# Performance work log

Measured on AMD Instinct MI355X. Metric: run time of the kernel, lower is better.

Reference implementation:

```python
import jax, jax.numpy as jnp
import numpy as np

NT, C, B, N, H, E = 32768, 128, 64, 512, 4, 524288  # total nodes, channels, graphs, nodes/graph, heads, edges
DH = C // H
EPS = 1e-5


def batchnorm(x, g, b):
    # BatchNorm1d over the node dimension (training-mode batch statistics)
    m = x.mean(axis=0)
    v = x.var(axis=0)
    return (x - m) * jax.lax.rsqrt(v + EPS) * g + b


def setup_inputs() -> dict:
    key = jax.random.key(0)
    ks = jax.random.split(key, 8)
    s = 1.0 / np.sqrt(C)
    return dict(
        x=jax.random.normal(ks[0], (NT, C), jnp.float32),
        edge_index=jax.random.randint(ks[1], (2, E), 0, NT, dtype=jnp.int32),
        Wc=jax.random.normal(ks[2], (C, C), jnp.float32) * s,
        bc=jnp.zeros((C,), jnp.float32),
        in_proj_w=jax.random.normal(ks[3], (3 * C, C), jnp.float32) * s,
        in_proj_b=jnp.zeros((3 * C,), jnp.float32),
        out_proj_w=jax.random.normal(ks[4], (C, C), jnp.float32) * s,
        out_proj_b=jnp.zeros((C,), jnp.float32),
        gn1=jnp.ones((C,), jnp.float32), bn1=jnp.zeros((C,), jnp.float32),
        gn2=jnp.ones((C,), jnp.float32), bn2=jnp.zeros((C,), jnp.float32),
        gn3=jnp.ones((C,), jnp.float32), bn3=jnp.zeros((C,), jnp.float32),
        Wm1=jax.random.normal(ks[5], (2 * C, C), jnp.float32) * s,
        bm1=jnp.zeros((2 * C,), jnp.float32),
        Wm2=jax.random.normal(ks[6], (C, 2 * C), jnp.float32) / np.sqrt(2 * C),
        bm2=jnp.zeros((C,), jnp.float32),
    )


def reference(x, edge_index, Wc, bc, in_proj_w, in_proj_b, out_proj_w, out_proj_b,
              gn1, bn1, gn2, bn2, gn3, bn3, Wm1, bm1, Wm2, bm2):
    # --- local branch: mean-aggregation message passing + linear + residual + BN ---
    src, dst = edge_index[0], edge_index[1]
    agg = jax.ops.segment_sum(x[src], dst, num_segments=NT)            # [NT, C]
    cnt = jax.ops.segment_sum(jnp.ones((E, 1), x.dtype), dst, num_segments=NT)
    agg = agg / jnp.maximum(cnt, 1.0)
    h_local = agg @ Wc.T + bc + x                                       # dropout p=0 -> no-op
    h_local = batchnorm(h_local, gn1, bn1)

    # --- global branch: to_dense_batch (equal-size graphs -> reshape) + MHA ---
    hd = x.reshape(B, N, C)
    qkv = hd @ in_proj_w.T + in_proj_b                                  # [B, N, 3C]
    q, k, v = jnp.split(qkv, 3, axis=-1)
    q = q.reshape(B, N, H, DH).transpose(0, 2, 1, 3)                    # [B, H, N, DH]
    k = k.reshape(B, N, H, DH).transpose(0, 2, 1, 3)
    v = v.reshape(B, N, H, DH).transpose(0, 2, 1, 3)
    scores = jnp.einsum('bhqd,bhkd->bhqk', q, k) / np.sqrt(DH)          # [B, H, N, N]
    attn = jax.nn.softmax(scores, axis=-1)
    o = jnp.einsum('bhqk,bhkd->bhqd', attn, v)                          # [B, H, N, DH]
    o = o.transpose(0, 2, 1, 3).reshape(B, N, C)
    h_attn = (o @ out_proj_w.T + out_proj_b).reshape(NT, C) + x
    h_attn = batchnorm(h_attn, gn2, bn2)

    # --- combine + MLP + final norm ---
    out = h_local + h_attn
    out = out + (jax.nn.relu(out @ Wm1.T + bm1) @ Wm2.T + bm2)
    return batchnorm(out, gn3, bn3)
```

## Files before the change

kernel.cpp:

```cpp
#include <hip/hip_runtime.h>
#include <cstddef>

#define NT    32768
#define CCH   128
#define BB    64
#define NNODE 512
#define NHEAD 4
#define DHEAD 32
#define EE    524288
#define EPS   1e-5f
#define MAXDEG 96
#define CURPAD 16
#define SSLOT  8
#define EGRP  2048

typedef unsigned short u16;
typedef unsigned int   u32;
typedef __attribute__((ext_vector_type(8))) short short8;
typedef __attribute__((ext_vector_type(4))) short short4v;
typedef __attribute__((ext_vector_type(4))) float f32x4;

__device__ __forceinline__ float b2f(u32 w) { return __uint_as_float(w << 16); }
__device__ __forceinline__ u16 f2b(float f) {
    u32 u = __float_as_uint(f);
    u += 0x7FFF + ((u >> 16) & 1);
    return (u16)(u >> 16);
}

__global__ __launch_bounds__(256) void prep_kernel(const float* __restrict__ x,
                                                   const float* __restrict__ Wc,
                                                   const float* __restrict__ Wqkv,
                                                   const float* __restrict__ Wo,
                                                   const float* __restrict__ Wm1,
                                                   const float* __restrict__ Wm2,
                                                   u16* __restrict__ xb,
                                                   u16* __restrict__ Wcb,
                                                   u16* __restrict__ Wqkvb,
                                                   u16* __restrict__ Wob,
                                                   u16* __restrict__ Wm1b,
                                                   u16* __restrict__ Wm2b,
                                                   const int* __restrict__ ei,
                                                   int* __restrict__ cursor,
                                                   int* __restrict__ bucket) {
    if (blockIdx.x >= 2120) {
        int b2 = blockIdx.x - 2120;
        int k = b2 & 7;
        int g = b2 >> 3;
        int base_e = g * EGRP;
        for (int j = threadIdx.x; j < EGRP; j += 256) {
            int dst = ei[EE + base_e + j];
            if ((dst & 7) == k) {
                int src = ei[base_e + j];
                int pos = atomicAdd(cursor + dst * CURPAD, 1);
                if (pos < MAXDEG) bucket[dst * MAXDEG + pos] = src;
            }
        }
        return;
    }
    int r = blockIdx.x * 256 + threadIdx.x;
    const float* src; u16* dst;
    if (r < 524288) { src = x; dst = xb; }
    else if ((r -= 524288) < 2048) { src = Wc; dst = Wcb; }
    else if ((r -= 2048) < 6144) { src = Wqkv; dst = Wqkvb; }
    else if ((r -= 6144) < 2048) { src = Wo; dst = Wob; }
    else if ((r -= 2048) < 4096) { src = Wm1; dst = Wm1b; }
    else { r -= 4096; src = Wm2; dst = Wm2b; }
    size_t base = (size_t)r * 8;
    float4 a = *(const float4*)(src + base);
    float4 b = *(const float4*)(src + base + 4);
    uint4 u;
    u.x = (u32)f2b(a.x) | ((u32)f2b(a.y) << 16);
    u.y = (u32)f2b(a.z) | ((u32)f2b(a.w) << 16);
    u.z = (u32)f2b(b.x) | ((u32)f2b(b.y) << 16);
    u.w = (u32)f2b(b.z) | ((u32)f2b(b.w) << 16);
    *(uint4*)(dst + base) = u;
}

struct GemmSmem {
    u16 As[128 * 32];
    u16 Bs[128 * 32];
    u16 Cs[4][16 * 72];
    float csum[128];
    float csq[128];
};

template <bool RELU, int RESID, bool STATS>
__device__ __forceinline__ void gemm_body(u16* __restrict__ As, u16* __restrict__ Bs,
                                          u16* __restrict__ Cs0, float* __restrict__ csum,
                                          float* __restrict__ csq,
                                          const u16* __restrict__ A,
                                          const u16* __restrict__ W,
                                          const float* __restrict__ bias,
                                          const u16* __restrict__ residb,
                                          u16* __restrict__ outb, int ostride,
                                          float* __restrict__ sum, float* __restrict__ sumsq,
                                          int slotbase, int m0, int K) {
    int tid = threadIdx.x;
    int lane = tid & 63, wave = tid >> 6;
    int wm = (wave & 1) * 64, wn = (wave >> 1) * 64;
    int l15 = lane & 15, l4 = lane >> 4;
    u16* Csw = Cs0 + wave * (16 * 72);

    if (STATS) {
        if (tid < 128) { csum[tid] = 0.f; csq[tid] = 0.f; }
    }

    f32x4 zero = {0.f, 0.f, 0.f, 0.f};
    f32x4 acc[4][4];
#pragma unroll
    for (int i = 0; i < 4; ++i)
#pragma unroll
        for (int j = 0; j < 4; ++j) acc[i][j] = zero;

    int srow = tid >> 2;
    int scol = (tid & 3) * 8;

    int kIter = K >> 5;
    uint4 a0 = *(const uint4*)(A + (size_t)(m0 + srow) * K + scol);
    uint4 a1 = *(const uint4*)(A + (size_t)(m0 + srow + 64) * K + scol);
    uint4 b0 = *(const uint4*)(W + (size_t)srow * K + scol);
    uint4 b1 = *(const uint4*)(W + (size_t)(srow + 64) * K + scol);
    for (int ki = 0; ki < kIter; ++ki) {
        if (ki) __syncthreads();
        *(uint4*)&As[srow * 32 + scol] = a0;
        *(uint4*)&As[(srow + 64) * 32 + scol] = a1;
        *(uint4*)&Bs[srow * 32 + scol] = b0;
        *(uint4*)&Bs[(srow + 64) * 32 + scol] = b1;
        if (ki + 1 < kIter) {
            int k0 = (ki + 1) * 32;
            a0 = *(const uint4*)(A + (size_t)(m0 + srow) * K + k0 + scol);
            a1 = *(const uint4*)(A + (size_t)(m0 + srow + 64) * K + k0 + scol);
            b0 = *(const uint4*)(W + (size_t)srow * K + k0 + scol);
            b1 = *(const uint4*)(W + (size_t)(srow + 64) * K + k0 + scol);
        }
        __syncthreads();
        short8 af[4], bf[4];
#pragma unroll
        for (int t = 0; t < 4; ++t) {
            af[t] = *(const short8*)&As[(wm + t * 16 + l15) * 32 + l4 * 8];
            bf[t] = *(const short8*)&Bs[(wn + t * 16 + l15) * 32 + l4 * 8];
        }
#pragma unroll
        for (int mt = 0; mt < 4; ++mt)
#pragma unroll
            for (int nt = 0; nt < 4; ++nt)
                acc[mt][nt] = __builtin_amdgcn_mfma_f32_16x16x32_bf16(af[mt], bf[nt], acc[mt][nt], 0, 0, 0);
    }

    float ps[4] = {0.f, 0.f, 0.f, 0.f};
    float pq[4] = {0.f, 0.f, 0.f, 0.f};
    int rl = lane >> 3;
    int cg = lane & 7;
#pragma unroll
    for (int mt = 0; mt < 4; ++mt) {
#pragma unroll
        for (int nt = 0; nt < 4; ++nt) {
            int lcol = wn + nt * 16 + l15;
            float bs = bias[lcol];
#pragma unroll
            for (int r = 0; r < 4; ++r) {
                int row = m0 + wm + mt * 16 + l4 * 4 + r;
                float v = acc[mt][nt][r] + bs;
                if (RESID == 2) v += b2f(residb[(size_t)row * 128 + lcol]);
                if (RELU) v = fmaxf(v, 0.0f);
                Csw[(l4 * 4 + r) * 72 + nt * 16 + l15] = f2b(v);
                if (STATS) { ps[nt] += v; pq[nt] += v * v; }
            }
        }
#pragma unroll
        for (int p = 0; p < 2; ++p) {
            int lrow = p * 8 + rl;
            uint4 wv = *(const uint4*)&Csw[lrow * 72 + cg * 8];
            int grow = m0 + wm + mt * 16 + lrow;
            *(uint4*)(outb + (size_t)grow * ostride + wn + cg * 8) = wv;
        }
    }
    if (STATS) {
#pragma unroll
        for (int nt = 0; nt < 4; ++nt) {
            atomicAdd(&csum[wn + nt * 16 + l15], ps[nt]);
            atomicAdd(&csq[wn + nt * 16 + l15], pq[nt]);
        }
        __syncthreads();
        if (tid < 128) {
            atomicAdd(sum + slotbase + tid, csum[tid]);
            atomicAdd(sumsq + slotbase + tid, csq[tid]);
        }
    }
}

__global__ __launch_bounds__(256) void gemm_wc_qkv(const int* __restrict__ bucket,
                                                   const int* __restrict__ cursor,
                                                   const u16* __restrict__ Wcb,
                                                   const float* __restrict__ bc,
                                                   const u16* __restrict__ xb,
                                                   u16* __restrict__ aggb,
                                                   u16* __restrict__ hlocb,
                                                   float* __restrict__ sum1,
                                                   float* __restrict__ sq1,
                                                   const u16* __restrict__ Wqkvb,
                                                   const float* __restrict__ bqkv,
                                                   u16* __restrict__ qkvb) {
    __shared__ GemmSmem sm;
    int y = blockIdx.y;
    int m0 = blockIdx.x * 128;
    int tid = threadIdx.x;

    if (y != 0) {
        gemm_body<false, 0, false>(sm.As, sm.Bs, &sm.Cs[0][0], sm.csum, sm.csq,
                                   xb, Wqkvb + (size_t)(y - 1) * 16384,
                                   bqkv + (y - 1) * 128, nullptr,
                                   qkvb + (y - 1) * 128, 384, nullptr, nullptr, 0, m0, 128);
        return;
    }

    {
        int (*srcs)[MAXDEG] = reinterpret_cast<int (*)[MAXDEG]>(sm.As);
        int ln = tid >> 4;
        int c8 = tid & 15;
        const u16* xp = xb + c8 * 8;
        for (int pass = 0; pass < 8; ++pass) {
            int n = pass * 16 + ln;
            int gn = m0 + n;
            int d = min(cursor[gn * CURPAD], MAXDEG);
            for (int j = c8; j < d; j += 16) srcs[ln][j] = bucket[gn * MAXDEG + j];
            __syncthreads();
            float s[8] = {0.f, 0.f, 0.f, 0.f, 0.f, 0.f, 0.f, 0.f};
            for (int base = 0; base < d; base += 8) {
                uint4 w[8];
#pragma unroll
                for (int u = 0; u < 8; ++u) {
                    int jj = base + u;
                    int idx = srcs[ln][jj < d ? jj : 0];
                    w[u] = *(const uint4*)(xp + (size_t)idx * CCH);
                }
#pragma unroll
                for (int u = 0; u < 8; ++u) {
                    if (base + u >= d) { w[u].x = 0; w[u].y = 0; w[u].z = 0; w[u].w = 0; }
                    s[0] += b2f(w[u].x & 0xffffu);
                    s[1] += b2f(w[u].x >> 16);
                    s[2] += b2f(w[u].y & 0xffffu);
                    s[3] += b2f(w[u].y >> 16);
                    s[4] += b2f(w[u].z & 0xffffu);
                    s[5] += b2f(w[u].z >> 16);
                    s[6] += b2f(w[u].w & 0xffffu);
                    s[7] += b2f(w[u].w >> 16);
                }
            }
            float inv = 1.0f / fmaxf((float)d, 1.0f);
            uint4 out;
            out.x = (u32)f2b(s[0] * inv) | ((u32)f2b(s[1] * inv) << 16);
            out.y = (u32)f2b(s[2] * inv) | ((u32)f2b(s[3] * inv) << 16);
            out.z = (u32)f2b(s[4] * inv) | ((u32)f2b(s[5] * inv) << 16);
            out.w = (u32)f2b(s[6] * inv) | ((u32)f2b(s[7] * inv) << 16);
            *(uint4*)(aggb + (size_t)gn * CCH + c8 * 8) = out;
            __syncthreads();
        }
    }
    __syncthreads();

    gemm_body<false, 2, true>(sm.As, sm.Bs, &sm.Cs[0][0], sm.csum, sm.csq,
                              aggb, Wcb, bc, xb, hlocb, 128, sum1, sq1,
                              (blockIdx.x & (SSLOT - 1)) << 7, m0, 128);
}

__global__ __launch_bounds__(256) void gemm_wo(const u16* __restrict__ ob,
                                               const u16* __restrict__ Wob,
                                               const float* __restrict__ bo,
                                               const u16* __restrict__ xb,
                                               u16* __restrict__ t2b,
                                               float* __restrict__ sum2, float* __restrict__ sq2) {
    __shared__ GemmSmem sm;
    gemm_body<false, 2, true>(sm.As, sm.Bs, &sm.Cs[0][0], sm.csum, sm.csq,
                              ob, Wob, bo, xb, t2b, 128, sum2, sq2,
                              (blockIdx.x & (SSLOT - 1)) << 7, blockIdx.x * 128, 128);
}

__global__ __launch_bounds__(256) void gemm_mlp2(const u16* __restrict__ hidb,
                                                 const u16* __restrict__ Wm2b,
                                                 const float* __restrict__ bm2,
                                                 const u16* __restrict__ shb,
                                                 u16* __restrict__ out2b,
                                                 float* __restrict__ sum3, float* __restrict__ sq3) {
    __shared__ GemmSmem sm;
    gemm_body<false, 2, true>(sm.As, sm.Bs, &sm.Cs[0][0], sm.csum, sm.csq,
                              hidb, Wm2b, bm2, shb, out2b, 128, sum3, sq3,
                              (blockIdx.x & (SSLOT - 1)) << 7, blockIdx.x * 128, 256);
}

__global__ __launch_bounds__(256) void gemm_m1c(const u16* __restrict__ hlocb,
                                                const u16* __restrict__ t2b,
                                                const float* __restrict__ sum1,
                                                const float* __restrict__ sq1,
                                                const float* __restrict__ g1,
                                                const float* __restrict__ bt1,
                                                const float* __restrict__ sum2,
                                                const float* __restrict__ sq2,
                                                const float* __restrict__ g2,
                                                const float* __restrict__ bt2,
                                                u16* __restrict__ shb,
                                                const u16* __restrict__ Wm1b,
                                                const float* __restrict__ bm1,
                                                u16* __restrict__ hidb) {
    __shared__ u16 As[128 * 32];
    __shared__ u16 Bs[128 * 32];
    __shared__ u16 Cs[4][16 * 72];
    __shared__ float AF1[128], BF1[128], AF2[128], BF2[128];
    int tid = threadIdx.x;
    {
        int c = tid & 127;
        const float* sm = (tid < 128) ? sum1 : sum2;
        const float* sq = (tid < 128) ? sq1 : sq2;
        const float* g  = (tid < 128) ? g1 : g2;
        const float* bt = (tid < 128) ? bt1 : bt2;
        float s = 0.f, q = 0.f;
#pragma unroll
        for (int sl = 0; sl < SSLOT; ++sl) { s += sm[sl * 128 + c]; q += sq[sl * 128 + c]; }
        float m = s * (1.0f / NT);
        float v = q * (1.0f / NT) - m * m;
        float a = g[c] * rsqrtf(v + EPS);
        if (tid < 128) { AF1[c] = a; BF1[c] = bt[c] - m * a; }
        else           { AF2[c] = a; BF2[c] = bt[c] - m * a; }
    }
    int m0 = blockIdx.x * 128, n0 = blockIdx.y * 128;
    int lane = tid & 63, wave = tid >> 6;
    int wm = (wave & 1) * 64, wn = (wave >> 1) * 64;
    int l15 = lane & 15, l4 = lane >> 4;

    f32x4 zero = {0.f, 0.f, 0.f, 0.f};
    f32x4 acc[4][4];
#pragma unroll
    for (int i = 0; i < 4; ++i)
#pragma unroll
        for (int j = 0; j < 4; ++j) acc[i][j] = zero;

    int srow = tid >> 2;
    int scol = (tid & 3) * 8;
    bool wr = (blockIdx.y == 0);

    uint4 h0 = *(const uint4*)(hlocb + (size_t)(m0 + srow) * 128 + scol);
    uint4 h1 = *(const uint4*)(hlocb + (size_t)(m0 + srow + 64) * 128 + scol);
    uint4 t0 = *(const uint4*)(t2b + (size_t)(m0 + srow) * 128 + scol);
    uint4 t1 = *(const uint4*)(t2b + (size_t)(m0 + srow + 64) * 128 + scol);
    uint4 b0 = *(const uint4*)(Wm1b + (size_t)(n0 + srow) * 128 + scol);
    uint4 b1 = *(const uint4*)(Wm1b + (size_t)(n0 + srow + 64) * 128 + scol);
    __syncthreads();
    for (int ki = 0; ki < 4; ++ki) {
        int k0 = ki * 32;
        if (ki) __syncthreads();
        uint4 c0, c1;
        {
            const u32 hw[4] = {h0.x, h0.y, h0.z, h0.w};
            const u32 tw[4] = {t0.x, t0.y, t0.z, t0.w};
            u32 ow[4];
#pragma unroll
            for (int p = 0; p < 4; ++p) {
                int cc = k0 + scol + p * 2;
                float v0 = AF1[cc] * b2f(hw[p] & 0xffffu) + BF1[cc] + AF2[cc] * b2f(tw[p] & 0xffffu) + BF2[cc];
                float v1 = AF1[cc + 1] * b2f(hw[p] >> 16) + BF1[cc + 1] + AF2[cc + 1] * b2f(tw[p] >> 16) + BF2[cc + 1];
                ow[p] = (u32)f2b(v0) | ((u32)f2b(v1) << 16);
            }
            c0.x = ow[0]; c0.y = ow[1]; c0.z = ow[2]; c0.w = ow[3];
        }
        {
            const u32 hw[4] = {h1.x, h1.y, h1.z, h1.w};
            const u32 tw[4] = {t1.x, t1.y, t1.z, t1.w};
            u32 ow[4];
#pragma unroll
            for (int p = 0; p < 4; ++p) {
                int cc = k0 + scol + p * 2;
                float v0 = AF1[cc] * b2f(hw[p] & 0xffffu) + BF1[cc] + AF2[cc] * b2f(tw[p] & 0xffffu) + BF2[cc];
                float v1 = AF1[cc + 1] * b2f(hw[p] >> 16) + BF1[cc + 1] + AF2[cc + 1] * b2f(tw[p] >> 16) + BF2[cc + 1];
                ow[p] = (u32)f2b(v0) | ((u32)f2b(v1) << 16);
            }
            c1.x = ow[0]; c1.y = ow[1]; c1.z = ow[2]; c1.w = ow[3];
        }
        *(uint4*)&As[srow * 32 + scol] = c0;
        *(uint4*)&As[(srow + 64) * 32 + scol] = c1;
        *(uint4*)&Bs[srow * 32 + scol] = b0;
        *(uint4*)&Bs[(srow + 64) * 32 + scol] = b1;
        if (wr) {
            *(uint4*)(shb + (size_t)(m0 + srow) * 128 + k0 + scol) = c0;
            *(uint4*)(shb + (size_t)(m0 + srow + 64) * 128 + k0 + scol) = c1;
        }
        if (ki < 3) {
            int kn = k0 + 32;
            h0 = *(const uint4*)(hlocb + (size_t)(m0 + srow) * 128 + kn + scol);
            h1 = *(const uint4*)(hlocb + (size_t)(m0 + srow + 64) * 128 + kn + scol);
            t0 = *(const uint4*)(t2b + (size_t)(m0 + srow) * 128 + kn + scol);
            t1 = *(const uint4*)(t2b + (size_t)(m0 + srow + 64) * 128 + kn + scol);
            b0 = *(const uint4*)(Wm1b + (size_t)(n0 + srow) * 128 + kn + scol);
            b1 = *(const uint4*)(Wm1b + (size_t)(n0 + srow + 64) * 128 + kn + scol);
        }
        __syncthreads();
        short8 af[4], bf[4];
#pragma unroll
        for (int t = 0; t < 4; ++t) {
            af[t] = *(const short8*)&As[(wm + t * 16 + l15) * 32 + l4 * 8];
            bf[t] = *(const short8*)&Bs[(wn + t * 16 + l15) * 32 + l4 * 8];
        }
#pragma unroll
        for (int mt = 0; mt < 4; ++mt)
#pragma unroll
            for (int nt = 0; nt < 4; ++nt)
                acc[mt][nt] = __builtin_amdgcn_mfma_f32_16x16x32_bf16(af[mt], bf[nt], acc[mt][nt], 0, 0, 0);
    }

    int rl = lane >> 3;
    int cg = lane & 7;
#pragma unroll
    for (int mt = 0; mt < 4; ++mt) {
#pragma unroll
        for (int nt = 0; nt < 4; ++nt) {
            int col = n0 + wn + nt * 16 + l15;
            float bs = bm1[col];
#pragma unroll
            for (int r = 0; r < 4; ++r) {
                float v = fmaxf(acc[mt][nt][r] + bs, 0.0f);
                Cs[wave][(l4 * 4 + r) * 72 + nt * 16 + l15] = f2b(v);
            }
        }
#pragma unroll
        for (int p = 0; p < 2; ++p) {
            int lrow = p * 8 + rl;
            uint4 wv = *(const uint4*)&Cs[wave][lrow * 72 + cg * 8];
            int grow = m0 + wm + mt * 16 + lrow;
            *(uint4*)(hidb + (size_t)grow * 256 + n0 + wn + cg * 8) = wv;
        }
    }
}

__global__ __launch_bounds__(256) void final_bn(const u16* __restrict__ X,
                                                const float* __restrict__ sum3,
                                                const float* __restrict__ sq3,
                                                const float* __restrict__ g3,
                                                const float* __restrict__ bt3,
                                                float* __restrict__ outp) {
    __shared__ float A3[128], B3[128];
    int t = threadIdx.x;
    if (t < 128) {
        float s = 0.f, q = 0.f;
#pragma unroll
        for (int sl = 0; sl < SSLOT; ++sl) { s += sum3[sl * 128 + t]; q += sq3[sl * 128 + t]; }
        float m = s * (1.0f / NT);
        float v = q * (1.0f / NT) - m * m;
        float a = g3[t] * rsqrtf(v + EPS);
        A3[t] = a;
        B3[t] = bt3[t] - m * a;
    }
    __syncthreads();
    int i8 = blockIdx.x * 256 + t;
    size_t i = (size_t)i8 * 8;
    int c = (int)(i & (CCH - 1));
    uint4 u = *(const uint4*)(X + i);
    float x[8];
    x[0] = b2f(u.x & 0xffffu); x[1] = b2f(u.x >> 16);
    x[2] = b2f(u.y & 0xffffu); x[3] = b2f(u.y >> 16);
    x[4] = b2f(u.z & 0xffffu); x[5] = b2f(u.z >> 16);
    x[6] = b2f(u.w & 0xffffu); x[7] = b2f(u.w >> 16);
    float4 o0, o1;
    o0.x = A3[c + 0] * x[0] + B3[c + 0];
    o0.y = A3[c + 1] * x[1] + B3[c + 1];
    o0.z = A3[c + 2] * x[2] + B3[c + 2];
    o0.w = A3[c + 3] * x[3] + B3[c + 3];
    o1.x = A3[c + 4] * x[4] + B3[c + 4];
    o1.y = A3[c + 5] * x[5] + B3[c + 5];
    o1.z = A3[c + 6] * x[6] + B3[c + 6];
    o1.w = A3[c + 7] * x[7] + B3[c + 7];
    *(float4*)(outp + i) = o0;
    *(float4*)(outp + i + 4) = o1;
}

__global__ __launch_bounds__(512) void attn_mfma(const u16* __restrict__ qkv,
                                                 u16* __restrict__ o) {
    __shared__ __align__(16) u16 Ks[512 * 40];
    __shared__ __align__(16) u16 Vt[32 * 520];
    int bh = blockIdx.x;
    int b = bh >> 2, h = bh & 3;
    int tid = threadIdx.x;
    int lane = tid & 63, wave = tid >> 6;
    int quad = lane >> 4, l15 = lane & 15;
    const float scale = 0.1767766952966369f;

    const u16* kvbase = qkv + (size_t)b * 512 * 384 + 128 + h * 32;
    for (int idx = tid; idx < 2048; idx += 512) {
        int row = idx >> 2, c = idx & 3;
        *(uint4*)&Ks[row * 40 + c * 8] = *(const uint4*)(kvbase + (size_t)row * 384 + c * 8);
    }
    for (int idx = tid; idx < 2048; idx += 512) {
        int row = idx >> 2, c = idx & 3;
        uint4 u = *(const uint4*)(kvbase + 128 + (size_t)row * 384 + c * 8);
        u16 e[8];
        *(uint4*)e = u;
#pragma unroll
        for (int i = 0; i < 8; ++i) Vt[(c * 8 + i) * 520 + row] = e[i];
    }
    __syncthreads();

    f32x4 zero = {0.f, 0.f, 0.f, 0.f};
    for (int qt = 0; qt < 4; ++qt) {
        int qbase = wave * 64 + qt * 16;
        short8 qf = *(const short8*)(qkv + (size_t)(b * 512 + qbase + l15) * 384 + h * 32 + quad * 8);
        float lq = 0.f;
        f32x4 oa[2] = {zero, zero};

        for (int kv0 = 0; kv0 < 512; kv0 += 64) {
            f32x4 s[4];
#pragma unroll
            for (int t = 0; t < 4; ++t) {
                short8 kb = *(const short8*)&Ks[(kv0 + t * 16 + l15) * 40 + quad * 8];
                s[t] = __builtin_amdgcn_mfma_f32_16x16x32_bf16(kb, qf, zero, 0, 0, 0);
            }
            short8 pp[2];
#pragma unroll
            for (int t = 0; t < 4; ++t) {
                float p0 = __expf(s[t][0] * scale);
                float p1 = __expf(s[t][1] * scale);
                float p2 = __expf(s[t][2] * scale);
                float p3 = __expf(s[t][3] * scale);
                lq += (p0 + p1) + (p2 + p3);
                int hi = (t & 1) * 4;
                pp[t >> 1][hi + 0] = (short)f2b(p0);
                pp[t >> 1][hi + 1] = (short)f2b(p1);
                pp[t >> 1][hi + 2] = (short)f2b(p2);
                pp[t >> 1][hi + 3] = (short)f2b(p3);
            }
#pragma unroll
            for (int tp = 0; tp < 2; ++tp) {
                int tb = kv0 + tp * 32;
#pragma unroll
                for (int n = 0; n < 2; ++n) {
                    const u16* vrow = &Vt[(n * 16 + l15) * 520 + tb + quad * 4];
                    short4v va = *(const short4v*)vrow;
                    short4v vb2 = *(const short4v*)(vrow + 16);
                    short8 vv = {va.x, va.y, va.z, va.w, vb2.x, vb2.y, vb2.z, vb2.w};
                    oa[n] = __builtin_amdgcn_mfma_f32_16x16x32_bf16(pp[tp], vv, oa[n], 0, 0, 0);
                }
            }
        }
        lq += __shfl_xor(lq, 16);
        lq += __shfl_xor(lq, 32);
        u16* op = o + (size_t)(b * 512 + qbase) * 128 + h * 32;
#pragma unroll
        for (int r = 0; r < 4; ++r) {
            float Lr = __shfl(lq, quad * 4 + r);
            float inv = 1.0f / Lr;
#pragma unroll
            for (int n = 0; n < 2; ++n)
                op[(quad * 4 + r) * 128 + n * 16 + l15] = f2b(oa[n][r] * inv);
        }
    }
}

extern "C" void kernel_launch(void* const* d_in, const int* in_sizes, int n_in,
                              void* d_out, int out_size, void* d_ws, size_t ws_size,
                              hipStream_t stream) {
    const float* x    = (const float*)d_in[0];
    const int*   ei   = (const int*)d_in[1];
    const float* Wc   = (const float*)d_in[2];
    const float* bc   = (const float*)d_in[3];
    const float* Wqkv = (const float*)d_in[4];
    const float* bqkv = (const float*)d_in[5];
    const float* Wo   = (const float*)d_in[6];
    const float* bo   = (const float*)d_in[7];
    const float* gn1  = (const float*)d_in[8];
    const float* bn1b = (const float*)d_in[9];
    const float* gn2  = (const float*)d_in[10];
    const float* bn2b = (const float*)d_in[11];
    const float* gn3  = (const float*)d_in[12];
    const float* bn3b = (const float*)d_in[13];
    const float* Wm1  = (const float*)d_in[14];
    const float* bm1  = (const float*)d_in[15];
    const float* Wm2  = (const float*)d_in[16];
    const float* bm2  = (const float*)d_in[17];
    float* outp = (float*)d_out;

    char* w = (char*)d_ws;
    const size_t MB = 1024 * 1024;
    u16* xb    = (u16*)(w);
    u16* hlocb = (u16*)(w + 8 * MB);
    u16* t2b   = (u16*)(w + 16 * MB);
    u16* out2b = (u16*)(w + 24 * MB);
    u16* qkvb  = (u16*)(w + 32 * MB);
    u16* hidb  = (u16*)(w + 56 * MB);
    u16* shb   = (u16*)(w + 72 * MB);
    int* bucket = (int*)(w + 80 * MB);
    int* cursor = (int*)(w + 92 * MB);
    float* stats = (float*)(w + 94 * MB);
    u16* Wcb   = (u16*)(w + 95 * MB);
    u16* Wqkvb = Wcb + 16384;
    u16* Wob   = Wqkvb + 49152;
    u16* Wm1b  = Wob + 16384;
    u16* Wm2b  = Wm1b + 32768;
    u16* ob    = (u16*)(w + 96 * MB);
    float* sum1 = stats;                  float* sq1 = stats + 1024;
    float* sum2 = stats + 2048;           float* sq2 = stats + 3072;
    float* sum3 = stats + 4096;           float* sq3 = stats + 5120;

    hipMemsetAsync(cursor, 0, 2 * MB + 6 * 1024 * 4, stream);

    prep_kernel<<<2120 + 2048, 256, 0, stream>>>(x, Wc, Wqkv, Wo, Wm1, Wm2,
                                                 xb, Wcb, Wqkvb, Wob, Wm1b, Wm2b,
                                                 ei, cursor, bucket);

    {
        dim3 g(NT / 128, 4);
        gemm_wc_qkv<<<g, 256, 0, stream>>>(bucket, cursor, Wcb, bc, xb, shb, hlocb, sum1, sq1,
                                           Wqkvb, bqkv, qkvb);
    }

    attn_mfma<<<BB * NHEAD, 512, 0, stream>>>(qkvb, ob);

    gemm_wo<<<NT / 128, 256, 0, stream>>>(ob, Wob, bo, xb, t2b, sum2, sq2);

    {
        dim3 g(NT / 128, 2);
        gemm_m1c<<<g, 256, 0, stream>>>(hlocb, t2b, sum1, sq1, gn1, bn1b,
                                        sum2, sq2, gn2, bn2b, shb, Wm1b, bm1, hidb);
    }

    gemm_mlp2<<<NT / 128, 256, 0, stream>>>(hidb, Wm2b, bm2, shb, out2b, sum3, sq3);

    final_bn<<<NT * CCH / 8 / 256, 256, 0, stream>>>(out2b, sum3, sq3, gn3, bn3b, outp);
}
```

Measured before the change: 232.7 us.

## Co-schedule attention with neighbor aggregation and Wc GEMM in one launch

```diff
diff --git a/kernel.cpp b/kernel.cpp
--- a/kernel.cpp
+++ b/kernel.cpp
@@ -189,33 +189,122 @@
     }
 }
 
-__global__ __launch_bounds__(256) void gemm_wc_qkv(const int* __restrict__ bucket,
-                                                   const int* __restrict__ cursor,
-                                                   const u16* __restrict__ Wcb,
-                                                   const float* __restrict__ bc,
-                                                   const u16* __restrict__ xb,
-                                                   u16* __restrict__ aggb,
-                                                   u16* __restrict__ hlocb,
-                                                   float* __restrict__ sum1,
-                                                   float* __restrict__ sq1,
-                                                   const u16* __restrict__ Wqkvb,
-                                                   const float* __restrict__ bqkv,
-                                                   u16* __restrict__ qkvb) {
+__global__ __launch_bounds__(256) void gemm_qkv(const u16* __restrict__ xb,
+                                                const u16* __restrict__ Wqkvb,
+                                                const float* __restrict__ bqkv,
+                                                u16* __restrict__ qkvb) {
     __shared__ GemmSmem sm;
     int y = blockIdx.y;
-    int m0 = blockIdx.x * 128;
+    gemm_body<false, 0, false>(sm.As, sm.Bs, &sm.Cs[0][0], sm.csum, sm.csq,
+                               xb, Wqkvb + (size_t)y * 16384, bqkv + y * 128, nullptr,
+                               qkvb + y * 128, 384, nullptr, nullptr, 0, blockIdx.x * 128, 128);
+}
+
+struct K3Smem {
+    union {
+        struct { u16 Ks[512 * 40]; u16 Vt[32 * 520]; } a;
+        GemmSmem g;
+    };
+};
+
+__global__ __launch_bounds__(256) void attn_gwc(const u16* __restrict__ qkv,
+                                                u16* __restrict__ o,
+                                                const int* __restrict__ bucket,
+                                                const int* __restrict__ cursor,
+                                                const u16* __restrict__ Wcb,
+                                                const float* __restrict__ bc,
+                                                const u16* __restrict__ xb,
+                                                u16* __restrict__ aggb,
+                                                u16* __restrict__ hlocb,
+                                                float* __restrict__ sum1,
+                                                float* __restrict__ sq1) {
+    __shared__ __align__(16) K3Smem sm;
+    int bid = blockIdx.x;
     int tid = threadIdx.x;
 
-    if (y != 0) {
-        gemm_body<false, 0, false>(sm.As, sm.Bs, &sm.Cs[0][0], sm.csum, sm.csq,
-                                   xb, Wqkvb + (size_t)(y - 1) * 16384,
-                                   bqkv + (y - 1) * 128, nullptr,
-                                   qkvb + (y - 1) * 128, 384, nullptr, nullptr, 0, m0, 128);
+    if (bid < 256) {
+        u16* Ks = sm.a.Ks;
+        u16* Vt = sm.a.Vt;
+        int b = bid >> 2, h = bid & 3;
+        int lane = tid & 63, wave = tid >> 6;
+        int quad = lane >> 4, l15 = lane & 15;
+        const float scale = 0.1767766952966369f;
+
+        const u16* kvbase = qkv + (size_t)b * 512 * 384 + 128 + h * 32;
+        for (int idx = tid; idx < 2048; idx += 256) {
+            int row = idx >> 2, c = idx & 3;
+            *(uint4*)&Ks[row * 40 + c * 8] = *(const uint4*)(kvbase + (size_t)row * 384 + c * 8);
+        }
+        for (int idx = tid; idx < 2048; idx += 256) {
+            int row = idx >> 2, c = idx & 3;
+            uint4 u = *(const uint4*)(kvbase + 128 + (size_t)row * 384 + c * 8);
+            u16 e[8];
+            *(uint4*)e = u;
+#pragma unroll
+            for (int i = 0; i < 8; ++i) Vt[(c * 8 + i) * 520 + row] = e[i];
+        }
+        __syncthreads();
+
+        f32x4 zero = {0.f, 0.f, 0.f, 0.f};
+        for (int qt = 0; qt < 8; ++qt) {
+            int qbase = wave * 128 + qt * 16;
+            short8 qf = *(const short8*)(qkv + (size_t)(b * 512 + qbase + l15) * 384 + h * 32 + quad * 8);
+            float lq = 0.f;
+            f32x4 oa[2] = {zero, zero};
+
+            for (int kv0 = 0; kv0 < 512; kv0 += 64) {
+                f32x4 s[4];
+#pragma unroll
+                for (int t = 0; t < 4; ++t) {
+                    short8 kb = *(const short8*)&Ks[(kv0 + t * 16 + l15) * 40 + quad * 8];
+                    s[t] = __builtin_amdgcn_mfma_f32_16x16x32_bf16(kb, qf, zero, 0, 0, 0);
+                }
+                short8 pp[2];
+#pragma unroll
+                for (int t = 0; t < 4; ++t) {
+                    float p0 = __expf(s[t][0] * scale);
+                    float p1 = __expf(s[t][1] * scale);
+                    float p2 = __expf(s[t][2] * scale);
+                    float p3 = __expf(s[t][3] * scale);
+                    lq += (p0 + p1) + (p2 + p3);
+                    int hi = (t & 1) * 4;
+                    pp[t >> 1][hi + 0] = (short)f2b(p0);
+                    pp[t >> 1][hi + 1] = (short)f2b(p1);
+                    pp[t >> 1][hi + 2] = (short)f2b(p2);
+                    pp[t >> 1][hi + 3] = (short)f2b(p3);
+                }
+#pragma unroll
+                for (int tp = 0; tp < 2; ++tp) {
+                    int tb = kv0 + tp * 32;
+#pragma unroll
+                    for (int n = 0; n < 2; ++n) {
+                        const u16* vrow = &Vt[(n * 16 + l15) * 520 + tb + quad * 4];
+                        short4v va = *(const short4v*)vrow;
+                        short4v vb2 = *(const short4v*)(vrow + 16);
+                        short8 vv = {va.x, va.y, va.z, va.w, vb2.x, vb2.y, vb2.z, vb2.w};
+                        oa[n] = __builtin_amdgcn_mfma_f32_16x16x32_bf16(pp[tp], vv, oa[n], 0, 0, 0);
+                    }
+                }
+            }
+            lq += __shfl_xor(lq, 16);
+            lq += __shfl_xor(lq, 32);
+            u16* op = o + (size_t)(b * 512 + qbase) * 128 + h * 32;
+#pragma unroll
+            for (int r = 0; r < 4; ++r) {
+                float Lr = __shfl(lq, quad * 4 + r);
+                float inv = 1.0f / Lr;
+#pragma unroll
+                for (int n = 0; n < 2; ++n)
+                    op[(quad * 4 + r) * 128 + n * 16 + l15] = f2b(oa[n][r] * inv);
+            }
+        }
         return;
     }
 
+    int m0 = (bid - 256) * 128;
+
     {
-        int (*srcs)[MAXDEG] = reinterpret_cast<int (*)[MAXDEG]>(sm.As);
+        int (*srcs)[MAXDEG] = reinterpret_cast<int (*)[MAXDEG]>(sm.g.As);
         int ln = tid >> 4;
         int c8 = tid & 15;
         const u16* xp = xb + c8 * 8;
@@ -259,9 +348,9 @@
     }
     __syncthreads();
 
-    gemm_body<false, 2, true>(sm.As, sm.Bs, &sm.Cs[0][0], sm.csum, sm.csq,
+    gemm_body<false, 2, true>(sm.g.As, sm.g.Bs, &sm.g.Cs[0][0], sm.g.csum, sm.g.csq,
                               aggb, Wcb, bc, xb, hlocb, 128, sum1, sq1,
-                              (blockIdx.x & (SSLOT - 1)) << 7, m0, 128);
+                              ((bid - 256) & (SSLOT - 1)) << 7, m0, 128);
 }
 
 __global__ __launch_bounds__(256) void gemm_wo(const u16* __restrict__ ob,
@@ -471,87 +560,6 @@
     *(float4*)(outp + i + 4) = o1;
 }
 
-__global__ __launch_bounds__(512) void attn_mfma(const u16* __restrict__ qkv,
-                                                 u16* __restrict__ o) {
-    __shared__ __align__(16) u16 Ks[512 * 40];
-    __shared__ __align__(16) u16 Vt[32 * 520];
-    int bh = blockIdx.x;
-    int b = bh >> 2, h = bh & 3;
-    int tid = threadIdx.x;
-    int lane = tid & 63, wave = tid >> 6;
-    int quad = lane >> 4, l15 = lane & 15;
-    const float scale = 0.1767766952966369f;
-
-    const u16* kvbase = qkv + (size_t)b * 512 * 384 + 128 + h * 32;
-    for (int idx = tid; idx < 2048; idx += 512) {
-        int row = idx >> 2, c = idx & 3;
-        *(uint4*)&Ks[row * 40 + c * 8] = *(const uint4*)(kvbase + (size_t)row * 384 + c * 8);
-    }
-    for (int idx = tid; idx < 2048; idx += 512) {
-        int row = idx >> 2, c = idx & 3;
-        uint4 u = *(const uint4*)(kvbase + 128 + (size_t)row * 384 + c * 8);
-        u16 e[8];
-        *(uint4*)e = u;
-#pragma unroll
-        for (int i = 0; i < 8; ++i) Vt[(c * 8 + i) * 520 + row] = e[i];
-    }
-    __syncthreads();
-
-    f32x4 zero = {0.f, 0.f, 0.f, 0.f};
-    for (int qt = 0; qt < 4; ++qt) {
-        int qbase = wave * 64 + qt * 16;
-        short8 qf = *(const short8*)(qkv + (size_t)(b * 512 + qbase + l15) * 384 + h * 32 + quad * 8);
-        float lq = 0.f;
-        f32x4 oa[2] = {zero, zero};
-
-        for (int kv0 = 0; kv0 < 512; kv0 += 64) {
-            f32x4 s[4];
-#pragma unroll
-            for (int t = 0; t < 4; ++t) {
-                short8 kb = *(const short8*)&Ks[(kv0 + t * 16 + l15) * 40 + quad * 8];
-                s[t] = __builtin_amdgcn_mfma_f32_16x16x32_bf16(kb, qf, zero, 0, 0, 0);
-            }
-            short8 pp[2];
-#pragma unroll
-            for (int t = 0; t < 4; ++t) {
-                float p0 = __expf(s[t][0] * scale);
-                float p1 = __expf(s[t][1] * scale);
-                float p2 = __expf(s[t][2] * scale);
-                float p3 = __expf(s[t][3] * scale);
-                lq += (p0 + p1) + (p2 + p3);
-                int hi = (t & 1) * 4;
-                pp[t >> 1][hi + 0] = (short)f2b(p0);
-                pp[t >> 1][hi + 1] = (short)f2b(p1);
-                pp[t >> 1][hi + 2] = (short)f2b(p2);
-                pp[t >> 1][hi + 3] = (short)f2b(p3);
-            }
-#pragma unroll
-            for (int tp = 0; tp < 2; ++tp) {
-                int tb = kv0 + tp * 32;
-#pragma unroll
-                for (int n = 0; n < 2; ++n) {
-                    const u16* vrow = &Vt[(n * 16 + l15) * 520 + tb + quad * 4];
-                    short4v va = *(const short4v*)vrow;
-                    short4v vb2 = *(const short4v*)(vrow + 16);
-                    short8 vv = {va.x, va.y, va.z, va.w, vb2.x, vb2.y, vb2.z, vb2.w};
-                    oa[n] = __builtin_amdgcn_mfma_f32_16x16x32_bf16(pp[tp], vv, oa[n], 0, 0, 0);
-                }
-            }
-        }
-        lq += __shfl_xor(lq, 16);
-        lq += __shfl_xor(lq, 32);
-        u16* op = o + (size_t)(b * 512 + qbase) * 128 + h * 32;
-#pragma unroll
-        for (int r = 0; r < 4; ++r) {
-            float Lr = __shfl(lq, quad * 4 + r);
-            float inv = 1.0f / Lr;
-#pragma unroll
-            for (int n = 0; n < 2; ++n)
-                op[(quad * 4 + r) * 128 + n * 16 + l15] = f2b(oa[n][r] * inv);
-        }
-    }
-}
-
 extern "C" void kernel_launch(void* const* d_in, const int* in_sizes, int n_in,
                               void* d_out, int out_size, void* d_ws, size_t ws_size,
                               hipStream_t stream) {
@@ -604,12 +612,12 @@
                                                  ei, cursor, bucket);
 
     {
-        dim3 g(NT / 128, 4);
-        gemm_wc_qkv<<<g, 256, 0, stream>>>(bucket, cursor, Wcb, bc, xb, shb, hlocb, sum1, sq1,
-                                           Wqkvb, bqkv, qkvb);
-    }
-
-    attn_mfma<<<BB * NHEAD, 512, 0, stream>>>(qkvb, ob);
+        dim3 g(NT / 128, 3);
+        gemm_qkv<<<g, 256, 0, stream>>>(xb, Wqkvb, bqkv, qkvb);
+    }
+
+    attn_gwc<<<512, 256, 0, stream>>>(qkvb, ob, bucket, cursor, Wcb, bc, xb,
+                                      shb , hlocb, sum1, sq1);
 
     gemm_wo<<<NT / 128, 256, 0, stream>>>(ob, Wob, bo, xb, t2b, sum2, sq2);
 
```

After: 222.9 us. 4.2% less time.
